# Kernel tuning notes

Hardware: AMD Instinct MI355X
Metric: run time of the kernel (lower is better)

## Reference

```python
import jax, jax.numpy as jnp
import numpy as np

BETA = 0.5

def setup_inputs() -> dict:
    key = jax.random.key(0)
    ks = jax.random.split(key, 12)
    B, H, d, hid = 2048, 100, 128, 256
    item_num, region_num, dist_num = 100000, 1000, 16
    return {
        "history": jax.random.randint(ks[0], (B, H), 0, item_num),
        "target": jax.random.randint(ks[1], (B,), 0, item_num),
        "history_region": jax.random.randint(ks[2], (B, H), 0, region_num),
        "target_region": jax.random.randint(ks[3], (B,), 0, region_num),
        "target_distance": jax.random.uniform(ks[4], (B,), dtype=jnp.float32),
        "E_hist": jax.random.normal(ks[5], (item_num, d), dtype=jnp.float32) * 0.01,
        "E_tgt": jax.random.normal(ks[6], (item_num, d), dtype=jnp.float32) * 0.01,
        "E_reg": jax.random.normal(ks[7], (region_num, d), dtype=jnp.float32) * 0.01,
        "E_dist": jax.random.normal(ks[8], (dist_num, d), dtype=jnp.float32) * 0.01,
        "W1": jax.random.normal(ks[9], (hid, 2 * d), dtype=jnp.float32) * 0.05,
        "b1": jnp.zeros((hid,), dtype=jnp.float32),
        "w2": jax.random.normal(ks[10], (hid,), dtype=jnp.float32) * 0.05,
    }

def reference(history, target, history_region, target_region, target_distance,
              E_hist, E_tgt, E_reg, E_dist, W1, b1, w2):
    # history embeddings: [B,H,2d]
    hist = jnp.concatenate([E_hist[history], E_reg[history_region]], axis=-1)
    # target embeddings: [B,1,2d]
    tgt = jnp.concatenate([E_tgt[target], E_reg[target_region]], axis=-1)[:, None, :]
    x = hist * tgt                                   # [B,H,2d]
    a = jax.nn.relu(jnp.einsum('bhd,kd->bhk', x, W1) + b1)  # [B,H,hid]
    score = jnp.einsum('bhk,k->bh', a, w2)           # [B,H]
    # distance bias: scalar per batch element
    dist = jnp.sum(target_distance[:, None] * E_dist[0], axis=1)  # [B]
    exp_A = jnp.exp(score + dist[:, None])           # [B,H]
    mask = (history != target[:, None]).astype(exp_A.dtype)
    exp_A = exp_A * mask
    exp_sum = jnp.power(jnp.sum(exp_A, axis=-1), BETA)  # [B]
    attn = exp_A / exp_sum[:, None]                  # [B,H]
    # weighted inner product: sum_h sum_d attn*hist*tgt
    pred = jnp.sum(hist * attn[:, :, None] * tgt, axis=(1, 2))  # [B]
    return jax.nn.sigmoid(pred)
```

## Files before the change

### kernel.cpp

```cpp
#include <hip/hip_runtime.h>
#include <stdint.h>

typedef __attribute__((ext_vector_type(8))) short bf16x8;
typedef __attribute__((ext_vector_type(4))) float f32x4;

#define HH  100
#define DD  128
#define HID 256

__device__ __forceinline__ unsigned short f2bf(float f) {
    unsigned int u = __float_as_uint(f);
    u += 0x7fffu + ((u >> 16) & 1u);
    return (unsigned short)(u >> 16);
}

__device__ __forceinline__ void load_lds_1k(const void* g, void* l) {
    __builtin_amdgcn_global_load_lds((const __attribute__((address_space(1))) unsigned int*)g,
                                     (__attribute__((address_space(3))) unsigned int*)l,
                                     16, 0, 0);
}

__global__ void w1_pack(const float* __restrict__ W1, unsigned short* __restrict__ W1p) {
    int unit = blockIdx.x * 256 + threadIdx.x;
    int lane = unit & 63;
    int s    = (unit >> 6) & 7;
    int st   = unit >> 9;
    int col  = lane & 15, quad = lane >> 4;
    const float* src = W1 + (size_t)(st * 16 + col) * HID + s * 32 + quad * 8;
    union { unsigned short u[8]; bf16x8 v; } o;
    #pragma unroll
    for (int j = 0; j < 8; j++) o.u[j] = f2bf(src[j]);
    *(bf16x8*)(W1p + (size_t)unit * 8) = o.v;
}

__global__ __launch_bounds__(512, 4) void nais_kernel(
    const int* __restrict__ history,
    const int* __restrict__ target,
    const int* __restrict__ history_region,
    const int* __restrict__ target_region,
    const float* __restrict__ target_distance,
    const float* __restrict__ E_hist,
    const float* __restrict__ E_tgt,
    const float* __restrict__ E_reg,
    const float* __restrict__ E_dist,
    const float* __restrict__ b1,
    const float* __restrict__ w2,
    const unsigned short* __restrict__ W1p,
    float* __restrict__ out)
{
    __shared__ __align__(16) unsigned short Bs[2][8192];
    __shared__ __align__(16) float tgts[HID];
    __shared__ __align__(16) float b1s[HID];
    __shared__ __align__(16) float w2s[HID];
    __shared__ float score[128];
    __shared__ float xsum[128];
    __shared__ float eA[HH];
    __shared__ float exs[HH];
    __shared__ int hidx[HH];
    __shared__ int hreg[HH];
    __shared__ float s_sumE;

    const int b    = blockIdx.x;
    const int t    = threadIdx.x;
    const int lane = t & 63;
    const int wave = t >> 6;
    const int col  = lane & 15;
    const int quad = lane >> 4;

    const int   tg    = target[b];
    const float tdist = target_distance[b];

    if (t < HH) {
        hidx[t] = history[b * HH + t];
        hreg[t] = history_region[b * HH + t];
    }
    if (wave == 4) {
        float4 v;
        if (lane < 32) v = *(const float4*)(E_tgt + (size_t)tg * DD + lane * 4);
        else           v = *(const float4*)(E_reg + (size_t)target_region[b] * DD + (lane - 32) * 4);
        *(float4*)(tgts + lane * 4) = v;
    }
    if (wave == 5) {
        *(float4*)(b1s + lane * 4) = *(const float4*)(b1 + lane * 4);
        *(float4*)(w2s + lane * 4) = *(const float4*)(w2 + lane * 4);
    }
    if (wave == 6) {
        float v = E_dist[lane] + E_dist[64 + lane];
        #pragma unroll
        for (int off = 32; off; off >>= 1) v += __shfl_xor(v, off);
        if (lane == 0) s_sumE = v;
    }
    __syncthreads();

    {
        const char* g = (const char*)W1p + wave * 2048 + lane * 16;
        char*       l = (char*)&Bs[0][0] + wave * 2048;
        load_lds_1k(g, l);
        load_lds_1k(g + 1024, l + 1024);
    }

    const int row = wave * 16 + col;
    const int rc  = (row < HH) ? row : row - 64;
    const int ih  = hidx[rc];
    const int ir  = hreg[rc];
    const float* ph = E_hist + (size_t)ih * DD + quad * 8;
    const float* pr = E_reg  + (size_t)ir * DD + quad * 8;
    bf16x8 afrag[8];
    float acc = 0.f;
    #pragma unroll
    for (int c = 0; c < 2; c++) {
        #pragma unroll
        for (int si = 0; si < 4; si++) {
            const int s = c * 4 + si;
            const float* src = (s < 4) ? (ph + s * 32) : (pr + (s - 4) * 32);
            float4 v0 = *(const float4*)src;
            float4 v1 = *(const float4*)(src + 4);
            const float* tp = tgts + s * 32 + quad * 8;
            float4 t0 = *(const float4*)tp, t1 = *(const float4*)(tp + 4);
            float x0 = v0.x * t0.x, x1 = v0.y * t0.y, x2 = v0.z * t0.z, x3 = v0.w * t0.w;
            float x4 = v1.x * t1.x, x5 = v1.y * t1.y, x6 = v1.z * t1.z, x7 = v1.w * t1.w;
            acc += (x0 + x1) + (x2 + x3) + ((x4 + x5) + (x6 + x7));
            union { unsigned short u[8]; bf16x8 v; } fb;
            fb.u[0] = f2bf(x0); fb.u[1] = f2bf(x1); fb.u[2] = f2bf(x2); fb.u[3] = f2bf(x3);
            fb.u[4] = f2bf(x4); fb.u[5] = f2bf(x5); fb.u[6] = f2bf(x6); fb.u[7] = f2bf(x7);
            afrag[s] = fb.v;
        }
        asm volatile("" ::: "memory");
    }
    {
        float v = acc;
        v += __shfl_xor(v, 16);
        v += __shfl_xor(v, 32);
        if (quad == 0) xsum[row] = v;
    }

    float sacc[4] = {};
    #pragma unroll 1
    for (int k = 0; k < 8; k++) {
        __syncthreads();
        if (k < 7) {
            const char* g = (const char*)W1p + (k + 1) * 16384 + wave * 2048 + lane * 16;
            char*       l = (char*)&Bs[(k + 1) & 1][0] + wave * 2048;
            load_lds_1k(g, l);
            load_lds_1k(g + 1024, l + 1024);
        }
        const unsigned short* buf = &Bs[k & 1][0];
        #pragma unroll
        for (int sti = 0; sti < 2; sti++) {
            const int st = k * 2 + sti;
            const float bb = b1s[st * 16 + col];
            const float ww = w2s[st * 16 + col];
            f32x4 acc0 = {0.f, 0.f, 0.f, 0.f};
            #pragma unroll
            for (int s = 0; s < 8; s++) {
                bf16x8 bfrag = *(const bf16x8*)(buf + ((sti * 8 + s) * 64 + lane) * 8);
                acc0 = __builtin_amdgcn_mfma_f32_16x16x32_bf16(afrag[s], bfrag, acc0, 0, 0, 0);
            }
            #pragma unroll
            for (int r = 0; r < 4; r++) {
                float z = acc0[r] + bb;
                sacc[r] += (z > 0.f) ? z * ww : 0.f;
            }
        }
    }
    #pragma unroll
    for (int r = 0; r < 4; r++) {
        float z = sacc[r];
        z += __shfl_xor(z, 1);
        z += __shfl_xor(z, 2);
        z += __shfl_xor(z, 4);
        z += __shfl_xor(z, 8);
        sacc[r] = z;
    }
    if (col == 0) {
        #pragma unroll
        for (int r = 0; r < 4; r++)
            score[wave * 16 + quad * 4 + r] = sacc[r];
    }

    __syncthreads();

    const float dist = tdist * s_sumE;
    if (t < HH) {
        float e = (hidx[t] != tg) ? expf(score[t] + dist) : 0.f;
        eA[t]  = e;
        exs[t] = e * xsum[t];
    }
    __syncthreads();
    if (t < 64) {
        float s1 = eA[t]  + ((t + 64 < HH) ? eA[t + 64]  : 0.f);
        float s2 = exs[t] + ((t + 64 < HH) ? exs[t + 64] : 0.f);
        #pragma unroll
        for (int off = 32; off; off >>= 1) {
            s1 += __shfl_xor(s1, off);
            s2 += __shfl_xor(s2, off);
        }
        if (t == 0) {
            float pred = s2 / sqrtf(s1);
            out[b] = 1.f / (1.f + expf(-pred));
        }
    }
}

extern "C" void kernel_launch(void* const* d_in, const int* in_sizes, int n_in,
                              void* d_out, int out_size, void* d_ws, size_t ws_size,
                              hipStream_t stream) {
    const int*   history         = (const int*)d_in[0];
    const int*   target          = (const int*)d_in[1];
    const int*   history_region  = (const int*)d_in[2];
    const int*   target_region   = (const int*)d_in[3];
    const float* target_distance = (const float*)d_in[4];
    const float* E_hist          = (const float*)d_in[5];
    const float* E_tgt           = (const float*)d_in[6];
    const float* E_reg           = (const float*)d_in[7];
    const float* E_dist          = (const float*)d_in[8];
    const float* W1              = (const float*)d_in[9];
    const float* b1              = (const float*)d_in[10];
    const float* w2              = (const float*)d_in[11];

    unsigned short* W1p = (unsigned short*)d_ws;
    const int B = in_sizes[1];

    w1_pack<<<32, 256, 0, stream>>>(W1, W1p);
    nais_kernel<<<B, 512, 0, stream>>>(history, target, history_region, target_region,
                                       target_distance, E_hist, E_tgt, E_reg, E_dist,
                                       b1, w2, W1p, (float*)d_out);
}
```

Baseline: 193.4 us.

## Keep W1 slices in registers per wave and stage activations in LDS

The work is reorganised so that each wave holds a fixed 32-column slice of W1 in registers, loaded directly from global memory. Activation row tiles are written as bf16 into LDS and shared across all waves. Before, each wave kept its own activation rows in registers and W1 was streamed through double-buffered LDS with a barrier per k-step. The new scheme removes the eight barriers and cuts the row tiles from 8 to 7, skipping the padding wave. In exchange it needs a per-wave partial-score buffer with a final cross-wave sum, more LDS (about 56KB for activations), and 16 bf16x8 register fragments per lane, all of which may lower occupancy.

```diff
diff --git a/kernel.cpp b/kernel.cpp
--- a/kernel.cpp
+++ b/kernel.cpp
@@ -12,12 +12,6 @@
     unsigned int u = __float_as_uint(f);
     u += 0x7fffu + ((u >> 16) & 1u);
     return (unsigned short)(u >> 16);
-}
-
-__device__ __forceinline__ void load_lds_1k(const void* g, void* l) {
-    __builtin_amdgcn_global_load_lds((const __attribute__((address_space(1))) unsigned int*)g,
-                                     (__attribute__((address_space(3))) unsigned int*)l,
-                                     16, 0, 0);
 }
 
 __global__ void w1_pack(const float* __restrict__ W1, unsigned short* __restrict__ W1p) {
@@ -48,12 +42,12 @@
     const unsigned short* __restrict__ W1p,
     float* __restrict__ out)
 {
-    __shared__ __align__(16) unsigned short Bs[2][8192];
+    __shared__ __align__(16) unsigned short As[7 * 4096];
+    __shared__ __align__(16) float scorep[8][112];
     __shared__ __align__(16) float tgts[HID];
     __shared__ __align__(16) float b1s[HID];
     __shared__ __align__(16) float w2s[HID];
-    __shared__ float score[128];
-    __shared__ float xsum[128];
+    __shared__ float xsum[112];
     __shared__ float eA[HH];
     __shared__ float exs[HH];
     __shared__ int hidx[HH];
@@ -92,97 +86,87 @@
     }
     __syncthreads();
 
-    {
-        const char* g = (const char*)W1p + wave * 2048 + lane * 16;
-        char*       l = (char*)&Bs[0][0] + wave * 2048;
-        load_lds_1k(g, l);
-        load_lds_1k(g + 1024, l + 1024);
-    }
-
-    const int row = wave * 16 + col;
-    const int rc  = (row < HH) ? row : row - 64;
-    const int ih  = hidx[rc];
-    const int ir  = hreg[rc];
-    const float* ph = E_hist + (size_t)ih * DD + quad * 8;
-    const float* pr = E_reg  + (size_t)ir * DD + quad * 8;
-    bf16x8 afrag[8];
-    float acc = 0.f;
-    #pragma unroll
-    for (int c = 0; c < 2; c++) {
-        #pragma unroll
-        for (int si = 0; si < 4; si++) {
-            const int s = c * 4 + si;
-            const float* src = (s < 4) ? (ph + s * 32) : (pr + (s - 4) * 32);
-            float4 v0 = *(const float4*)src;
-            float4 v1 = *(const float4*)(src + 4);
-            const float* tp = tgts + s * 32 + quad * 8;
-            float4 t0 = *(const float4*)tp, t1 = *(const float4*)(tp + 4);
-            float x0 = v0.x * t0.x, x1 = v0.y * t0.y, x2 = v0.z * t0.z, x3 = v0.w * t0.w;
-            float x4 = v1.x * t1.x, x5 = v1.y * t1.y, x6 = v1.z * t1.z, x7 = v1.w * t1.w;
-            acc += (x0 + x1) + (x2 + x3) + ((x4 + x5) + (x6 + x7));
-            union { unsigned short u[8]; bf16x8 v; } fb;
-            fb.u[0] = f2bf(x0); fb.u[1] = f2bf(x1); fb.u[2] = f2bf(x2); fb.u[3] = f2bf(x3);
-            fb.u[4] = f2bf(x4); fb.u[5] = f2bf(x5); fb.u[6] = f2bf(x6); fb.u[7] = f2bf(x7);
-            afrag[s] = fb.v;
-        }
-        asm volatile("" ::: "memory");
-    }
-    {
+    if (wave < 7) {
+        const int row = wave * 16 + col;
+        const int rc  = (row < HH) ? row : row - 64;
+        const int ih  = hidx[rc];
+        const int ir  = hreg[rc];
+        const float* ph = E_hist + (size_t)ih * DD + quad * 8;
+        const float* pr = E_reg  + (size_t)ir * DD + quad * 8;
+        unsigned short* ap = As + (size_t)wave * 4096;
+        float acc = 0.f;
+        #pragma unroll
+        for (int c = 0; c < 2; c++) {
+            #pragma unroll
+            for (int si = 0; si < 4; si++) {
+                const int s = c * 4 + si;
+                const float* src = (s < 4) ? (ph + s * 32) : (pr + (s - 4) * 32);
+                float4 v0 = *(const float4*)src;
+                float4 v1 = *(const float4*)(src + 4);
+                const float* tp = tgts + s * 32 + quad * 8;
+                float4 t0 = *(const float4*)tp, t1 = *(const float4*)(tp + 4);
+                float x0 = v0.x * t0.x, x1 = v0.y * t0.y, x2 = v0.z * t0.z, x3 = v0.w * t0.w;
+                float x4 = v1.x * t1.x, x5 = v1.y * t1.y, x6 = v1.z * t1.z, x7 = v1.w * t1.w;
+                acc += (x0 + x1) + (x2 + x3) + ((x4 + x5) + (x6 + x7));
+                union { unsigned short u[8]; bf16x8 v; } fb;
+                fb.u[0] = f2bf(x0); fb.u[1] = f2bf(x1); fb.u[2] = f2bf(x2); fb.u[3] = f2bf(x3);
+                fb.u[4] = f2bf(x4); fb.u[5] = f2bf(x5); fb.u[6] = f2bf(x6); fb.u[7] = f2bf(x7);
+                *(bf16x8*)(ap + (size_t)(s * 64 + lane) * 8) = fb.v;
+            }
+            asm volatile("" ::: "memory");
+        }
         float v = acc;
         v += __shfl_xor(v, 16);
         v += __shfl_xor(v, 32);
         if (quad == 0) xsum[row] = v;
     }
 
-    float sacc[4] = {};
+    bf16x8 bfrag[16];
+    #pragma unroll
+    for (int i = 0; i < 16; i++) {
+        const int unit = ((2 * wave + (i >> 3)) * 8 + (i & 7)) * 64 + lane;
+        bfrag[i] = *(const bf16x8*)(W1p + (size_t)unit * 8);
+    }
+    __syncthreads();
+
+    const int st0 = 2 * wave;
+    const float bb0 = b1s[st0 * 16 + col],      ww0 = w2s[st0 * 16 + col];
+    const float bb1 = b1s[st0 * 16 + 16 + col], ww1 = w2s[st0 * 16 + 16 + col];
     #pragma unroll 1
-    for (int k = 0; k < 8; k++) {
-        __syncthreads();
-        if (k < 7) {
-            const char* g = (const char*)W1p + (k + 1) * 16384 + wave * 2048 + lane * 16;
-            char*       l = (char*)&Bs[(k + 1) & 1][0] + wave * 2048;
-            load_lds_1k(g, l);
-            load_lds_1k(g + 1024, l + 1024);
-        }
-        const unsigned short* buf = &Bs[k & 1][0];
-        #pragma unroll
-        for (int sti = 0; sti < 2; sti++) {
-            const int st = k * 2 + sti;
-            const float bb = b1s[st * 16 + col];
-            const float ww = w2s[st * 16 + col];
-            f32x4 acc0 = {0.f, 0.f, 0.f, 0.f};
-            #pragma unroll
-            for (int s = 0; s < 8; s++) {
-                bf16x8 bfrag = *(const bf16x8*)(buf + ((sti * 8 + s) * 64 + lane) * 8);
-                acc0 = __builtin_amdgcn_mfma_f32_16x16x32_bf16(afrag[s], bfrag, acc0, 0, 0, 0);
-            }
-            #pragma unroll
-            for (int r = 0; r < 4; r++) {
-                float z = acc0[r] + bb;
-                sacc[r] += (z > 0.f) ? z * ww : 0.f;
-            }
-        }
-    }
-    #pragma unroll
-    for (int r = 0; r < 4; r++) {
-        float z = sacc[r];
-        z += __shfl_xor(z, 1);
-        z += __shfl_xor(z, 2);
-        z += __shfl_xor(z, 4);
-        z += __shfl_xor(z, 8);
-        sacc[r] = z;
-    }
-    if (col == 0) {
-        #pragma unroll
-        for (int r = 0; r < 4; r++)
-            score[wave * 16 + quad * 4 + r] = sacc[r];
-    }
-
-    __syncthreads();
-
+    for (int i = 0; i < 7; i++) {
+        int mt = wave + i; if (mt >= 7) mt -= 7;
+        const unsigned short* ap = As + (size_t)mt * 4096;
+        f32x4 a0 = {0.f, 0.f, 0.f, 0.f}, a1 = {0.f, 0.f, 0.f, 0.f};
+        #pragma unroll
+        for (int s = 0; s < 8; s++) {
+            bf16x8 af = *(const bf16x8*)(ap + (size_t)(s * 64 + lane) * 8);
+            a0 = __builtin_amdgcn_mfma_f32_16x16x32_bf16(af, bfrag[s],     a0, 0, 0, 0);
+            a1 = __builtin_amdgcn_mfma_f32_16x16x32_bf16(af, bfrag[8 + s], a1, 0, 0, 0);
+        }
+        f32x4 sv;
+        #pragma unroll
+        for (int r = 0; r < 4; r++) {
+            float z0 = a0[r] + bb0;
+            float z1 = a1[r] + bb1;
+            float sres = ((z0 > 0.f) ? z0 * ww0 : 0.f) + ((z1 > 0.f) ? z1 * ww1 : 0.f);
+            sres += __shfl_xor(sres, 1);
+            sres += __shfl_xor(sres, 2);
+            sres += __shfl_xor(sres, 4);
+            sres += __shfl_xor(sres, 8);
+            sv[r] = sres;
+        }
+        if (col == 0) *(f32x4*)&scorep[wave][mt * 16 + quad * 4] = sv;
+    }
+    __syncthreads();
+
+    float sc = 0.f;
+    if (t < 112) {
+        #pragma unroll
+        for (int w = 0; w < 8; w++) sc += scorep[w][t];
+    }
     const float dist = tdist * s_sumE;
     if (t < HH) {
-        float e = (hidx[t] != tg) ? expf(score[t] + dist) : 0.f;
+        float e = (hidx[t] != tg) ? expf(sc + dist) : 0.f;
         eA[t]  = e;
         exs[t] = e * xsum[t];
     }
```

Measured after the change: 180.7 us. 6.6% less time.
